# Kernel tuning notes

Measured on AMD Instinct MI355X. Metric: run time of the kernel, lower is better.

## Reference

```python
import math
import jax, jax.numpy as jnp
import numpy as np

STRIDE = 8
IMG = 2048
NA = 9            # num anchors per cell (len(cfg['anchor_size']))
NC = 80           # num classes
TOPK = 1000
CONF = 0.05
NMS_T = 0.6
CTR_CLAMP = 32.0
EXP_CLAMP = math.log(1e8)            # DEFAULT_EXP_CLAMP
SCALE_CLAMP = math.log(1000.0 / 16)  # DEFAULT_SCALE_CLAMP


def setup_inputs() -> dict:
    key = jax.random.key(0)
    k1, k2, k3 = jax.random.split(key, 3)
    H = W = IMG // STRIDE  # 256
    obj_pred = jax.random.normal(k1, (1, NA, H, W), jnp.float32)
    cls_pred = jax.random.normal(k2, (1, NA * NC, H, W), jnp.float32)
    reg_pred = jax.random.normal(k3, (1, NA * 4, H, W), jnp.float32) * 0.5
    # generate_anchors: grid centers (+0.5)*stride, tiled anchor sizes -> [H*W*NA, 4] (cx,cy,w,h)
    ys, xs = jnp.meshgrid(jnp.arange(H), jnp.arange(W), indexing='ij')
    xy = (jnp.stack([xs, ys], -1).reshape(-1, 2).astype(jnp.float32) + 0.5) * STRIDE
    sizes = jnp.array([[32, 32], [64, 64], [128, 128], [32, 64], [64, 128],
                       [128, 256], [64, 32], [128, 64], [256, 128]], jnp.float32)
    anchor_boxes = jnp.concatenate(
        [jnp.repeat(xy[:, None, :], NA, axis=1),
         jnp.broadcast_to(sizes[None], (H * W, NA, 2))], axis=-1).reshape(-1, 4)
    return {"obj_pred": obj_pred, "cls_pred": cls_pred,
            "reg_pred": reg_pred, "anchor_boxes": anchor_boxes}


def _detect(obj_pred, cls_pred, reg_pred, anchor_boxes):
    B, _, H, W = obj_pred.shape
    obj = obj_pred.reshape(B, NA, 1, H, W)
    cls = cls_pred.reshape(B, NA, NC, H, W)
    # normalized_cls_pred = cls + obj - log(1 + exp(clamp(cls)) + exp(clamp(obj)))
    norm = cls + obj - jnp.log(1.0 + jnp.exp(jnp.minimum(cls, EXP_CLAMP))
                               + jnp.exp(jnp.minimum(obj, EXP_CLAMP)))
    norm = norm.transpose(0, 3, 4, 1, 2).reshape(B, -1, NC)[0]          # [M, NC]
    reg = reg_pred.reshape(B, NA, 4, H, W).transpose(0, 3, 4, 1, 2).reshape(B, -1, 4)[0]  # [M, 4]
    prob = jax.nn.sigmoid(norm)
    scores_all = prob.max(axis=-1)
    labels_all = prob.argmax(axis=-1)
    scores, idx = jax.lax.top_k(scores_all, TOPK)                        # descending
    labels = labels_all[idx]
    reg = reg[idx]
    anc = anchor_boxes[idx]
    # decode_boxes
    ctr_off = jnp.clip(reg[..., :2] * anc[..., 2:], -CTR_CLAMP, CTR_CLAMP)
    ctr = anc[..., :2] + ctr_off
    wh = anc[..., 2:] * jnp.exp(jnp.minimum(reg[..., 2:], SCALE_CLAMP))
    boxes = jnp.concatenate([ctr - 0.5 * wh, ctr + 0.5 * wh], axis=-1)
    boxes = jnp.clip(boxes / IMG, 0.0, 1.0)
    return scores, labels, boxes


def _nms_keep(scores, labels, boxes):
    # scores are sorted descending; per-class greedy NMS == class-masked global greedy NMS
    valid = scores >= CONF
    x1, y1, x2, y2 = boxes[:, 0], boxes[:, 1], boxes[:, 2], boxes[:, 3]
    areas = (x2 - x1) * (y2 - y1)
    xx1 = jnp.maximum(x1[:, None], x1[None, :])
    yy1 = jnp.maximum(y1[:, None], y1[None, :])
    xx2 = jnp.minimum(x2[:, None], x2[None, :])
    yy2 = jnp.minimum(y2[:, None], y2[None, :])
    inter = jnp.maximum(1e-28, xx2 - xx1) * jnp.maximum(1e-28, yy2 - yy1)
    iou = inter / (areas[:, None] + areas[None, :] - inter + 1e-14)      # [N, N]
    sup = (iou > NMS_T) & (labels[:, None] == labels[None, :])
    later = jnp.arange(TOPK)[None, :] > jnp.arange(TOPK)[:, None]

    def body(i, keep):
        row = sup[i] & later[i] & keep[i]   # i suppresses only if still kept
        return keep & ~row

    return jax.lax.fori_loop(0, TOPK, body, valid)


def reference(obj_pred, cls_pred, reg_pred, anchor_boxes):
    scores, labels, boxes = _detect(obj_pred, cls_pred, reg_pred, anchor_boxes)
    keep = _nms_keep(scores, labels, boxes)
    # fixed-shape outputs: detections sorted by score with a keep mask
    return scores, labels, boxes, keep
```

## Files before the change

### kernel.cpp

```cpp
#include <hip/hip_runtime.h>
#include <stdint.h>

#define NA 9
#define NC 80
#define NTOT 589824
#define TOPK 1000
#define CONF 0.05f
#define NMS_T 0.6
#define CTR_CLAMP 32.0
#define IMGF 2048.0
#define SCALE_CLAMP 4.135166556742356

#define BITS_OFF   0u
#define LABELS_OFF 2359296u
#define HIST_OFF   4718592u
#define CNT_OFF    4784128u
#define BARC_OFF   4784384u
#define FLAG_OFF   4790528u
#define CAND_OFF   4796672u
#define BOXES_OFF  4829440u
#define LABS_OFF   4845440u
#define SUPB_OFF   4849664u
#define ZERO_LEN   78080u

#define NBLK 500
#define SPIN_CAP 200000

__device__ __forceinline__ void stg32(unsigned* p, unsigned v) {
  __hip_atomic_store(p, v, __ATOMIC_RELAXED, __HIP_MEMORY_SCOPE_AGENT);
}
__device__ __forceinline__ unsigned ldg32(const unsigned* p) {
  return __hip_atomic_load((unsigned*)p, __ATOMIC_RELAXED, __HIP_MEMORY_SCOPE_AGENT);
}
__device__ __forceinline__ void stg64(unsigned long long* p, unsigned long long v) {
  __hip_atomic_store(p, v, __ATOMIC_RELAXED, __HIP_MEMORY_SCOPE_AGENT);
}
__device__ __forceinline__ unsigned long long ldg64(const unsigned long long* p) {
  return __hip_atomic_load((unsigned long long*)p, __ATOMIC_RELAXED,
                           __HIP_MEMORY_SCOPE_AGENT);
}

__device__ __forceinline__ unsigned* lslot(unsigned* base, int idx) {
  return (unsigned*)((char*)base + (size_t)idx * 256u);
}

__device__ __forceinline__ void barrier_sync(unsigned* cnts, unsigned* flags,
                                             int b, int bid, unsigned target,
                                             bool i_arrive) {
  __syncthreads();
  if (threadIdx.x == 0) {
    if (i_arrive)
      __hip_atomic_fetch_add(lslot(cnts, b * 8 + (bid & 7)), 1u, __ATOMIC_RELAXED,
                             __HIP_MEMORY_SCOPE_AGENT);
    if (bid == 0) {
      for (int it = 0; it < SPIN_CAP; it++) {
        unsigned s = 0;
#pragma unroll
        for (int i = 0; i < 8; i++)
          s += __hip_atomic_load(lslot(cnts, b * 8 + i), __ATOMIC_RELAXED,
                                 __HIP_MEMORY_SCOPE_AGENT);
        if (s >= target) break;
        __builtin_amdgcn_s_sleep(2);
      }
#pragma unroll
      for (int i = 0; i < 8; i++)
        __hip_atomic_store(lslot(flags, b * 8 + i), 1u, __ATOMIC_RELAXED,
                           __HIP_MEMORY_SCOPE_AGENT);
    } else {
      for (int it = 0; it < SPIN_CAP; it++) {
        if (__hip_atomic_load(lslot(flags, b * 8 + (bid & 7)), __ATOMIC_RELAXED,
                              __HIP_MEMORY_SCOPE_AGENT) != 0u)
          break;
        __builtin_amdgcn_s_sleep(2);
      }
    }
  }
  __syncthreads();
  asm volatile("" ::: "memory");
}

__device__ __forceinline__ float cexpf(float x) {
#pragma clang fp contract(off)
  float m = floorf(__builtin_fmaf(x, 1.44269504088896341f, 0.5f));
  float r = __builtin_fmaf(m, -0.693359375f, x);
  r = __builtin_fmaf(m, 2.12194440e-4f, r);
  float r2 = r * r;
  float y = 1.9875691500E-4f;
  y = __builtin_fmaf(y, r, 1.3981999507E-3f);
  y = __builtin_fmaf(y, r, 8.3334519073E-3f);
  y = __builtin_fmaf(y, r, 4.1665795894E-2f);
  y = __builtin_fmaf(y, r, 1.6666665459E-1f);
  y = __builtin_fmaf(y, r, 5.0000001201E-1f);
  y = __builtin_fmaf(y, r2, r) + 1.0f;
  return ldexpf(y, (int)m);
}

__device__ __forceinline__ float clogf_(float xin) {
#pragma clang fp contract(off)
  unsigned b = __float_as_uint(xin);
  int e = (int)(b >> 23) - 126;
  float m = __uint_as_float((b & 0x007FFFFFu) | 0x3F000000u);
  if (m < 0.707106781186547524f) { e -= 1; m = m + m; }
  float x = m - 1.0f;
  float z = x * x;
  float y = 7.0376836292E-2f;
  y = __builtin_fmaf(y, x, -1.1514610310E-1f);
  y = __builtin_fmaf(y, x, 1.1676998740E-1f);
  y = __builtin_fmaf(y, x, -1.2420140846E-1f);
  y = __builtin_fmaf(y, x, 1.4249322787E-1f);
  y = __builtin_fmaf(y, x, -1.6668057665E-1f);
  y = __builtin_fmaf(y, x, 2.0000714765E-1f);
  y = __builtin_fmaf(y, x, -2.4999993993E-1f);
  y = __builtin_fmaf(y, x, 3.3333331174E-1f);
  y = y * x * z;
  float ef = (float)e;
  y = __builtin_fmaf(ef, -2.12194440e-4f, y);
  y = __builtin_fmaf(-0.5f, z, y);
  float res = x + y;
  res = __builtin_fmaf(ef, 0.693359375f, res);
  return res;
}

__global__ __launch_bounds__(256) void k_score(const float4* __restrict__ obj4,
                                               const float4* __restrict__ cls4,
                                               unsigned* __restrict__ bits_all,
                                               int* __restrict__ labels_all,
                                               unsigned* __restrict__ hist) {
#pragma clang fp contract(off)
  __shared__ unsigned lh[16384];
  int tid = threadIdx.x;
  for (int b = tid; b < 16384; b += 256) lh[b] = 0u;
  __syncthreads();
  int t = blockIdx.x * 256 + tid;
  int a = t >> 14;
  int rem = t & 16383;
  float4 ov = obj4[t];
  float ob[4] = {ov.x, ov.y, ov.z, ov.w};
  float best[4] = {-1e30f, -1e30f, -1e30f, -1e30f};
  int bc[4] = {0, 0, 0, 0};
  const float4* cp = cls4 + a * 80 * 16384 + rem;
#pragma unroll 8
  for (int c = 0; c < 80; c++) {
    float4 cv = cp[c * 16384];
    float cl[4] = {cv.x, cv.y, cv.z, cv.w};
#pragma unroll
    for (int k = 0; k < 4; k++) {
      if (cl[k] > best[k]) { best[k] = cl[k]; bc[k] = c; }
    }
  }
  unsigned bv[4];
#pragma unroll
  for (int k = 0; k < 4; k++) {
    float c = best[k], o = ob[k];
    float ec = cexpf(c);
    float eo = cexpf(o);
    float L = clogf_((1.0f + ec) + eo);
    float nrm = (c + o) - L;
    float p = 1.0f / (1.0f + cexpf(-nrm));
    bv[k] = __float_as_uint(p);
    atomicAdd(&lh[bv[k] >> 16], 1u);
  }
  unsigned po = (unsigned)(a * 65536 + rem * 4);
#pragma unroll
  for (int k = 0; k < 4; k++) { bits_all[po + k] = bv[k]; labels_all[po + k] = bc[k]; }
  __syncthreads();
  for (int b = tid; b < 16384; b += 256) {
    unsigned v = lh[b];
    if (v) atomicAdd(&hist[b], v);
  }
}

__device__ __forceinline__ unsigned long long shflxor64(unsigned long long v, int m) {
  unsigned lo = __shfl_xor((unsigned)v, m, 64);
  unsigned hi = __shfl_xor((unsigned)(v >> 32), m, 64);
  return ((unsigned long long)hi << 32) | lo;
}

__global__ __launch_bounds__(256) void k_tail2(const unsigned* __restrict__ hist,
                                               const unsigned* __restrict__ bits_all,
                                               const int* __restrict__ labels_all,
                                               const float* __restrict__ reg_pred,
                                               const float* __restrict__ anchors,
                                               unsigned* __restrict__ cand_cnt,
                                               unsigned* __restrict__ barc,
                                               unsigned* __restrict__ flags,
                                               unsigned long long* __restrict__ cand,
                                               float* __restrict__ out,
                                               float* __restrict__ boxes_s,
                                               int* __restrict__ labels_s,
                                               unsigned long long* __restrict__ supB) {
  int tid = threadIdx.x;
  int bid = blockIdx.x;

  __shared__ __align__(16) char smem[20480];
  unsigned* s_cut = (unsigned*)smem;
  unsigned long long* s_key = (unsigned long long*)smem;
  float* s_bx = (float*)smem;
  int* s_lb = (int*)(smem + 16000);
  __shared__ int sC;
  __shared__ unsigned sAbove;
  __shared__ unsigned s_cutB;

  {
    unsigned base = (unsigned)tid * 64u;
    unsigned s = 0;
#pragma unroll 8
    for (int b = 0; b < 64; b++) s += hist[base + b];
    unsigned v = s;
    s_cut[tid] = v;
    __syncthreads();
    for (int off = 1; off < 256; off <<= 1) {
      unsigned add = (tid + off < 256) ? s_cut[tid + off] : 0u;
      __syncthreads();
      v += add;
      s_cut[tid] = v;
      __syncthreads();
    }
    unsigned nxt = (tid < 255) ? s_cut[tid + 1] : 0u;
    if (v >= TOPK && nxt < TOPK) { sC = tid; sAbove = nxt; }
    __syncthreads();
    int C = sC;
    unsigned above = sAbove;
    if (tid < 64) {
      unsigned h = hist[(unsigned)C * 64u + (unsigned)tid];
      unsigned acc = h;
      for (int off = 1; off < 64; off <<= 1) {
        unsigned o = __shfl_down(acc, off, 64);
        if (tid + off < 64) acc += o;
      }
      acc += above;
      if (acc >= TOPK && (tid == 63 || (acc - h) < TOPK))
        s_cutB = (unsigned)(C * 64 + tid);
    }
    __syncthreads();
  }
  unsigned cB = s_cutB;

  for (unsigned t = (unsigned)bid * 256u + (unsigned)tid; t < (unsigned)NTOT;
       t += (unsigned)(NBLK * 256)) {
    unsigned bits = bits_all[t];
    bool win = (bits >> 16) >= cB;
    unsigned long long m = __ballot(win);
    if (m != 0ull) {
      int lane = tid & 63;
      int leader = __ffsll((long long)m) - 1;
      unsigned base2 = 0;
      if (lane == leader) base2 = atomicAdd(cand_cnt, (unsigned)__popcll(m));
      base2 = __shfl(base2, leader, 64);
      if (win) {
        unsigned a = t >> 16;
        unsigned hw = t & 65535u;
        unsigned j = hw * 9u + a;
        unsigned pos = base2 + (unsigned)__popcll(m & ((1ull << lane) - 1ull));
        if (pos < 4096u)
          stg64(&cand[pos], ((unsigned long long)bits << 20) |
                                (unsigned long long)(0xFFFFFu - j));
      }
    }
  }
  barrier_sync(barc, flags, 0, bid, NBLK, true);

  if (bid < 16) {
    int c = bid * 256 + tid;
    unsigned M = ldg32(cand_cnt);
    if (M > 4096u) M = 4096u;
    unsigned long long mykey = (c < (int)M) ? ldg64(&cand[c]) : 0ull;
    unsigned rank = 0;
    int ntile = (int)((M + 255u) >> 8);
    for (int tile = 0; tile < ntile; tile++) {
      __syncthreads();
      int src = tile * 256 + tid;
      s_key[tid] = (src < (int)M) ? ldg64(&cand[src]) : 0ull;
      __syncthreads();
#pragma unroll 8
      for (int q = 0; q < 256; q++) rank += (s_key[q] > mykey) ? 1u : 0u;
    }
    if (c < (int)M && rank < TOPK) {
      int r = (int)rank;
      unsigned j = 0xFFFFFu - (unsigned)(mykey & 0xFFFFFull);
      unsigned hw = j / 9u;
      unsigned a = j - hw * 9u;
      int lab = labels_all[a * 65536u + hw];
      unsigned base = a * 4u * 65536u + hw;
      double r0 = (double)reg_pred[base];
      double r1 = (double)reg_pred[base + 65536u];
      double r2 = (double)reg_pred[base + 131072u];
      double r3 = (double)reg_pred[base + 196608u];
      double ax = (double)anchors[j * 4u + 0], ay = (double)anchors[j * 4u + 1];
      double aw = (double)anchors[j * 4u + 2], ah = (double)anchors[j * 4u + 3];
      double ox = fmin(fmax(r0 * aw, -CTR_CLAMP), CTR_CLAMP);
      double oy = fmin(fmax(r1 * ah, -CTR_CLAMP), CTR_CLAMP);
      double cx = ax + ox, cy = ay + oy;
      double ww = aw * exp(fmin(r2, SCALE_CLAMP));
      double hh = ah * exp(fmin(r3, SCALE_CLAMP));
      float x1 = (float)fmin(fmax((cx - 0.5 * ww) * (1.0 / IMGF), 0.0), 1.0);
      float y1 = (float)fmin(fmax((cy - 0.5 * hh) * (1.0 / IMGF), 0.0), 1.0);
      float x2 = (float)fmin(fmax((cx + 0.5 * ww) * (1.0 / IMGF), 0.0), 1.0);
      float y2 = (float)fmin(fmax((cy + 0.5 * hh) * (1.0 / IMGF), 0.0), 1.0);
      out[1000 + r] = (float)lab;
      out[2000 + 4 * r + 0] = x1;
      out[2000 + 4 * r + 1] = y1;
      out[2000 + 4 * r + 2] = x2;
      out[2000 + 4 * r + 3] = y2;
      stg32((unsigned*)&out[r], (unsigned)(mykey >> 20));
      stg32((unsigned*)&boxes_s[4 * r + 0], __float_as_uint(x1));
      stg32((unsigned*)&boxes_s[4 * r + 1], __float_as_uint(y1));
      stg32((unsigned*)&boxes_s[4 * r + 2], __float_as_uint(x2));
      stg32((unsigned*)&boxes_s[4 * r + 3], __float_as_uint(y2));
      stg32((unsigned*)&labels_s[r], (unsigned)lab);
    }
  }
  barrier_sync(barc, flags, 1, bid, 16, bid < 16);

  for (int t = tid; t < 4000; t += 256)
    s_bx[t] = __uint_as_float(ldg32((const unsigned*)&boxes_s[t]));
  for (int t = tid; t < 1000; t += 256)
    s_lb[t] = (int)ldg32((const unsigned*)&labels_s[t]);
  __syncthreads();
  for (int half = 0; half < 2; half++) {
    int i = bid + half * NBLK;
    double ix1 = (double)s_bx[4 * i], iy1 = (double)s_bx[4 * i + 1];
    double ix2 = (double)s_bx[4 * i + 2], iy2 = (double)s_bx[4 * i + 3];
    double ia = (ix2 - ix1) * (iy2 - iy1);
    int il = s_lb[i];
    for (int rep = 0; rep < 4; rep++) {
      int j = rep * 256 + tid;
      bool s = false;
      if (j < TOPK && j > i && s_lb[j] == il) {
        double jx1 = (double)s_bx[4 * j], jy1 = (double)s_bx[4 * j + 1];
        double jx2 = (double)s_bx[4 * j + 2], jy2 = (double)s_bx[4 * j + 3];
        double xx1 = fmax(ix1, jx1), yy1 = fmax(iy1, jy1);
        double xx2 = fmin(ix2, jx2), yy2 = fmin(iy2, jy2);
        double inter = fmax(1e-28, xx2 - xx1) * fmax(1e-28, yy2 - yy1);
        double ja = (jx2 - jx1) * (jy2 - jy1);
        double iou = inter / (ia + ja - inter + 1e-14);
        s = iou > NMS_T;
      }
      unsigned long long w = __ballot(s);
      if ((tid & 63) == 0)
        stg64(&supB[(rep * 4 + (tid >> 6)) * 1024 + i], w);
    }
  }
  __syncthreads();
  if (tid == 0)
    __hip_atomic_fetch_add(lslot(barc, 2 * 8 + (bid & 7)), 1u, __ATOMIC_RELAXED,
                           __HIP_MEMORY_SCOPE_AGENT);
  if (bid != 0) return;
  if (tid == 0) {
    for (int it = 0; it < SPIN_CAP; it++) {
      unsigned s = 0;
#pragma unroll
      for (int i = 0; i < 8; i++)
        s += __hip_atomic_load(lslot(barc, 2 * 8 + i), __ATOMIC_RELAXED,
                               __HIP_MEMORY_SCOPE_AGENT);
      if (s >= NBLK) break;
      __builtin_amdgcn_s_sleep(2);
    }
  }
  __syncthreads();
  asm volatile("" ::: "memory");

  if (tid < 64) {
    int lane = tid;
    float* keep_out = out + 6000;
    unsigned long long inval[16];
#pragma unroll
    for (int m = 0; m < 16; m++) {
      int j = m * 64 + lane;
      bool bad = (j >= TOPK) ||
                 (__uint_as_float(ldg32((const unsigned*)&out[j])) < CONF);
      inval[m] = __ballot(bad);
    }
    unsigned long long kept[16];
#pragma unroll
    for (int b = 0; b < 16; b++) {
      unsigned long long acc = 0ull;
#pragma unroll
      for (int m = 0; m < b; m++) {
        unsigned long long r = ldg64(&supB[b * 1024 + m * 64 + lane]);
        if ((kept[m] >> lane) & 1ull) acc |= r;
      }
      if (b > 0) {
#pragma unroll
        for (int s = 1; s < 64; s <<= 1) acc |= shflxor64(acc, s);
      }
      unsigned alo = __builtin_amdgcn_readfirstlane((unsigned)acc);
      unsigned ahi = __builtin_amdgcn_readfirstlane((unsigned)(acc >> 32));
      unsigned long long cur = inval[b] | (((unsigned long long)ahi << 32) | alo);
      unsigned long long diag = ldg64(&supB[b * 1024 + b * 64 + lane]);
      unsigned dlo = (unsigned)diag, dhi = (unsigned)(diag >> 32);
#pragma unroll 8
      for (int k = 0; k < 64; k++) {
        unsigned rlo = __builtin_amdgcn_readlane(dlo, k);
        unsigned rhi = __builtin_amdgcn_readlane(dhi, k);
        unsigned long long rk = ((unsigned long long)rhi << 32) | rlo;
        unsigned long long take = ((cur >> k) & 1ull) ? 0ull : rk;
        cur |= take;
      }
      kept[b] = ~cur;
    }
#pragma unroll
    for (int m = 0; m < 16; m++) {
      int j = m * 64 + lane;
      if (j < TOPK) keep_out[j] = ((kept[m] >> lane) & 1ull) ? 1.0f : 0.0f;
    }
  }
}

extern "C" void kernel_launch(void* const* d_in, const int* in_sizes, int n_in,
                              void* d_out, int out_size, void* d_ws, size_t ws_size,
                              hipStream_t stream) {
  const float* obj = (const float*)d_in[0];
  const float* cls = (const float*)d_in[1];
  const float* reg = (const float*)d_in[2];
  const float* anc = (const float*)d_in[3];
  float* out = (float*)d_out;
  char* ws = (char*)d_ws;

  unsigned* bits_all = (unsigned*)(ws + BITS_OFF);
  int* labels_all = (int*)(ws + LABELS_OFF);
  unsigned* hist = (unsigned*)(ws + HIST_OFF);
  unsigned* cand_cnt = (unsigned*)(ws + CNT_OFF);
  unsigned* barc = (unsigned*)(ws + BARC_OFF);
  unsigned* flags = (unsigned*)(ws + FLAG_OFF);
  unsigned long long* cand = (unsigned long long*)(ws + CAND_OFF);
  float* boxes_s = (float*)(ws + BOXES_OFF);
  int* labels_s = (int*)(ws + LABS_OFF);
  unsigned long long* supB = (unsigned long long*)(ws + SUPB_OFF);

  hipMemsetAsync(ws + HIST_OFF, 0, ZERO_LEN, stream);

  k_score<<<576, 256, 0, stream>>>((const float4*)obj, (const float4*)cls, bits_all,
                                   labels_all, hist);

  void* kargs[] = {(void*)&hist,     (void*)&bits_all, (void*)&labels_all,
                   (void*)&reg,      (void*)&anc,      (void*)&cand_cnt,
                   (void*)&barc,     (void*)&flags,    (void*)&cand,
                   (void*)&out,      (void*)&boxes_s,  (void*)&labels_s,
                   (void*)&supB};
  hipLaunchCooperativeKernel((const void*)k_tail2, dim3(NBLK), dim3(256), kargs, 0,
                             stream);
}
```

Baseline: 403.4 us.

## Fuse scoring, histogram zeroing and tail into one cooperative kernel

Merges the memset, the scoring and histogram kernel, and the cooperative top-k/NMS kernel into a single cooperative launch of 512 blocks. The scoring work moves into a grid-stride loop. Block 0 zeroes the histogram and barrier state in-kernel and publishes a magic flag that other blocks wait on before merging their histograms. The goal is to remove two launch gaps and the memset. In exchange the scoring phase runs on fewer resident blocks with an uneven second iteration, and the init flag persists across calls, which weakens the zeroing guarantee on later calls.

```diff
diff --git a/kernel.cpp b/kernel.cpp
--- a/kernel.cpp
+++ b/kernel.cpp
@@ -4,6 +4,7 @@
 #define NA 9
 #define NC 80
 #define NTOT 589824
+#define NT4  147456
 #define TOPK 1000
 #define CONF 0.05f
 #define NMS_T 0.6
@@ -16,15 +17,16 @@
 #define HIST_OFF   4718592u
 #define CNT_OFF    4784128u
 #define BARC_OFF   4784384u
-#define FLAG_OFF   4790528u
-#define CAND_OFF   4796672u
-#define BOXES_OFF  4829440u
-#define LABS_OFF   4845440u
-#define SUPB_OFF   4849664u
-#define ZERO_LEN   78080u
-
-#define NBLK 500
+#define FLAG_OFF   4792576u
+#define INITF_OFF  4800768u
+#define CAND_OFF   4802816u
+#define BOXES_OFF  4835584u
+#define LABS_OFF   4851584u
+#define SUPB_OFF   4855584u
+
+#define NBLK 512
 #define SPIN_CAP 200000
+#define INIT_MAGIC 0x9E3779B97F4A7C15ull
 
 __device__ __forceinline__ void stg32(unsigned* p, unsigned v) {
   __hip_atomic_store(p, v, __ATOMIC_RELAXED, __HIP_MEMORY_SCOPE_AGENT);
@@ -121,108 +123,121 @@
   return res;
 }
 
-__global__ __launch_bounds__(256) void k_score(const float4* __restrict__ obj4,
-                                               const float4* __restrict__ cls4,
-                                               unsigned* __restrict__ bits_all,
-                                               int* __restrict__ labels_all,
-                                               unsigned* __restrict__ hist) {
-#pragma clang fp contract(off)
-  __shared__ unsigned lh[16384];
-  int tid = threadIdx.x;
-  for (int b = tid; b < 16384; b += 256) lh[b] = 0u;
-  __syncthreads();
-  int t = blockIdx.x * 256 + tid;
-  int a = t >> 14;
-  int rem = t & 16383;
-  float4 ov = obj4[t];
-  float ob[4] = {ov.x, ov.y, ov.z, ov.w};
-  float best[4] = {-1e30f, -1e30f, -1e30f, -1e30f};
-  int bc[4] = {0, 0, 0, 0};
-  const float4* cp = cls4 + a * 80 * 16384 + rem;
-#pragma unroll 8
-  for (int c = 0; c < 80; c++) {
-    float4 cv = cp[c * 16384];
-    float cl[4] = {cv.x, cv.y, cv.z, cv.w};
-#pragma unroll
-    for (int k = 0; k < 4; k++) {
-      if (cl[k] > best[k]) { best[k] = cl[k]; bc[k] = c; }
-    }
-  }
-  unsigned bv[4];
-#pragma unroll
-  for (int k = 0; k < 4; k++) {
-    float c = best[k], o = ob[k];
-    float ec = cexpf(c);
-    float eo = cexpf(o);
-    float L = clogf_((1.0f + ec) + eo);
-    float nrm = (c + o) - L;
-    float p = 1.0f / (1.0f + cexpf(-nrm));
-    bv[k] = __float_as_uint(p);
-    atomicAdd(&lh[bv[k] >> 16], 1u);
-  }
-  unsigned po = (unsigned)(a * 65536 + rem * 4);
-#pragma unroll
-  for (int k = 0; k < 4; k++) { bits_all[po + k] = bv[k]; labels_all[po + k] = bc[k]; }
-  __syncthreads();
-  for (int b = tid; b < 16384; b += 256) {
-    unsigned v = lh[b];
-    if (v) atomicAdd(&hist[b], v);
-  }
-}
-
 __device__ __forceinline__ unsigned long long shflxor64(unsigned long long v, int m) {
   unsigned lo = __shfl_xor((unsigned)v, m, 64);
   unsigned hi = __shfl_xor((unsigned)(v >> 32), m, 64);
   return ((unsigned long long)hi << 32) | lo;
 }
 
-__global__ __launch_bounds__(256) void k_tail2(const unsigned* __restrict__ hist,
-                                               const unsigned* __restrict__ bits_all,
-                                               const int* __restrict__ labels_all,
-                                               const float* __restrict__ reg_pred,
-                                               const float* __restrict__ anchors,
-                                               unsigned* __restrict__ cand_cnt,
-                                               unsigned* __restrict__ barc,
-                                               unsigned* __restrict__ flags,
-                                               unsigned long long* __restrict__ cand,
-                                               float* __restrict__ out,
-                                               float* __restrict__ boxes_s,
-                                               int* __restrict__ labels_s,
-                                               unsigned long long* __restrict__ supB) {
+__global__ __launch_bounds__(256) void k_fused(
+    const float4* __restrict__ obj4, const float4* __restrict__ cls4,
+    unsigned* __restrict__ bits_all, int* __restrict__ labels_all,
+    unsigned* __restrict__ hist, const float* __restrict__ reg_pred,
+    const float* __restrict__ anchors, unsigned* __restrict__ cand_cnt,
+    unsigned* __restrict__ barc, unsigned* __restrict__ flags,
+    unsigned* __restrict__ initf, unsigned long long* __restrict__ cand,
+    float* __restrict__ out, float* __restrict__ boxes_s,
+    int* __restrict__ labels_s, unsigned long long* __restrict__ supB) {
   int tid = threadIdx.x;
   int bid = blockIdx.x;
 
-  __shared__ __align__(16) char smem[20480];
-  unsigned* s_cut = (unsigned*)smem;
-  unsigned long long* s_key = (unsigned long long*)smem;
-  float* s_bx = (float*)smem;
-  int* s_lb = (int*)(smem + 16000);
-  __shared__ int sC;
-  __shared__ unsigned sAbove;
-  __shared__ unsigned s_cutB;
-
+  __shared__ __align__(16) unsigned lh[16384];
+
+  for (int i = tid; i < 16384; i += 256) lh[i] = 0u;
+  if (bid == 0) {
+    for (int i = tid; i < 16384; i += 256) stg32(&hist[i], 0u);
+    if (tid == 0) stg32(cand_cnt, 0u);
+    if (tid < 32) {
+      stg32(lslot(barc, tid), 0u);
+      stg32(lslot(flags, tid), 0u);
+    }
+  }
+  __syncthreads();
+  if (bid == 0 && tid < 8)
+    stg64((unsigned long long*)lslot(initf, tid), INIT_MAGIC);
+
+  {
+#pragma clang fp contract(off)
+    for (unsigned t4 = (unsigned)bid * 256u + (unsigned)tid; t4 < (unsigned)NT4;
+         t4 += (unsigned)(NBLK * 256)) {
+      int a = (int)(t4 >> 14);
+      int rem = (int)(t4 & 16383u);
+      float4 ov = obj4[t4];
+      float ob[4] = {ov.x, ov.y, ov.z, ov.w};
+      float best[4] = {-1e30f, -1e30f, -1e30f, -1e30f};
+      int bc[4] = {0, 0, 0, 0};
+      const float4* cp = cls4 + a * 80 * 16384 + rem;
+#pragma unroll 8
+      for (int c = 0; c < 80; c++) {
+        float4 cv = cp[c * 16384];
+        float cl[4] = {cv.x, cv.y, cv.z, cv.w};
+#pragma unroll
+        for (int k = 0; k < 4; k++) {
+          if (cl[k] > best[k]) { best[k] = cl[k]; bc[k] = c; }
+        }
+      }
+      unsigned bv[4];
+#pragma unroll
+      for (int k = 0; k < 4; k++) {
+        float c = best[k], o = ob[k];
+        float ec = cexpf(c);
+        float eo = cexpf(o);
+        float L = clogf_((1.0f + ec) + eo);
+        float nrm = (c + o) - L;
+        float p = 1.0f / (1.0f + cexpf(-nrm));
+        bv[k] = __float_as_uint(p);
+        atomicAdd(&lh[bv[k] >> 16], 1u);
+      }
+      unsigned po = (unsigned)(a * 65536 + rem * 4);
+      stg64((unsigned long long*)&bits_all[po],
+            (unsigned long long)bv[0] | ((unsigned long long)bv[1] << 32));
+      stg64((unsigned long long*)&bits_all[po + 2],
+            (unsigned long long)bv[2] | ((unsigned long long)bv[3] << 32));
+      stg64((unsigned long long*)&labels_all[po],
+            (unsigned long long)(unsigned)bc[0] |
+                ((unsigned long long)(unsigned)bc[1] << 32));
+      stg64((unsigned long long*)&labels_all[po + 2],
+            (unsigned long long)(unsigned)bc[2] |
+                ((unsigned long long)(unsigned)bc[3] << 32));
+    }
+  }
+  __syncthreads();
+  if (tid == 0) {
+    for (int it = 0; it < SPIN_CAP; it++) {
+      if (ldg64((unsigned long long*)lslot(initf, bid & 7)) == INIT_MAGIC) break;
+      __builtin_amdgcn_s_sleep(2);
+    }
+  }
+  __syncthreads();
+  for (int b = tid; b < 16384; b += 256) {
+    unsigned v = lh[b];
+    if (v) atomicAdd(&hist[b], v);
+  }
+  barrier_sync(barc, flags, 0, bid, NBLK, true);
+
+  unsigned cB;
   {
     unsigned base = (unsigned)tid * 64u;
     unsigned s = 0;
 #pragma unroll 8
     for (int b = 0; b < 64; b++) s += hist[base + b];
     unsigned v = s;
-    s_cut[tid] = v;
+    lh[tid] = v;
     __syncthreads();
     for (int off = 1; off < 256; off <<= 1) {
-      unsigned add = (tid + off < 256) ? s_cut[tid + off] : 0u;
+      unsigned add = (tid + off < 256) ? lh[tid + off] : 0u;
       __syncthreads();
       v += add;
-      s_cut[tid] = v;
+      lh[tid] = v;
       __syncthreads();
     }
-    unsigned nxt = (tid < 255) ? s_cut[tid + 1] : 0u;
-    if (v >= TOPK && nxt < TOPK) { sC = tid; sAbove = nxt; }
+    unsigned nxt = (tid < 255) ? lh[tid + 1] : 0u;
+    if (v >= TOPK && nxt < TOPK) { lh[260] = (unsigned)tid; lh[261] = nxt; }
     __syncthreads();
-    int C = sC;
-    unsigned above = sAbove;
+    unsigned C = lh[260];
+    unsigned above = lh[261];
     if (tid < 64) {
-      unsigned h = hist[(unsigned)C * 64u + (unsigned)tid];
+      unsigned h = hist[C * 64u + (unsigned)tid];
       unsigned acc = h;
       for (int off = 1; off < 64; off <<= 1) {
         unsigned o = __shfl_down(acc, off, 64);
@@ -230,11 +245,11 @@
       }
       acc += above;
       if (acc >= TOPK && (tid == 63 || (acc - h) < TOPK))
-        s_cutB = (unsigned)(C * 64 + tid);
+        lh[262] = C * 64u + (unsigned)tid;
     }
     __syncthreads();
-  }
-  unsigned cB = s_cutB;
+    cB = lh[262];
+  }
 
   for (unsigned t = (unsigned)bid * 256u + (unsigned)tid; t < (unsigned)NTOT;
        t += (unsigned)(NBLK * 256)) {
@@ -258,9 +273,10 @@
       }
     }
   }
-  barrier_sync(barc, flags, 0, bid, NBLK, true);
+  barrier_sync(barc, flags, 1, bid, NBLK, true);
 
   if (bid < 16) {
+    unsigned long long* s_key = (unsigned long long*)lh;
     int c = bid * 256 + tid;
     unsigned M = ldg32(cand_cnt);
     if (M > 4096u) M = 4096u;
@@ -310,40 +326,46 @@
       stg32((unsigned*)&labels_s[r], (unsigned)lab);
     }
   }
-  barrier_sync(barc, flags, 1, bid, 16, bid < 16);
-
-  for (int t = tid; t < 4000; t += 256)
-    s_bx[t] = __uint_as_float(ldg32((const unsigned*)&boxes_s[t]));
-  for (int t = tid; t < 1000; t += 256)
-    s_lb[t] = (int)ldg32((const unsigned*)&labels_s[t]);
-  __syncthreads();
-  for (int half = 0; half < 2; half++) {
-    int i = bid + half * NBLK;
-    double ix1 = (double)s_bx[4 * i], iy1 = (double)s_bx[4 * i + 1];
-    double ix2 = (double)s_bx[4 * i + 2], iy2 = (double)s_bx[4 * i + 3];
-    double ia = (ix2 - ix1) * (iy2 - iy1);
-    int il = s_lb[i];
-    for (int rep = 0; rep < 4; rep++) {
-      int j = rep * 256 + tid;
-      bool s = false;
-      if (j < TOPK && j > i && s_lb[j] == il) {
-        double jx1 = (double)s_bx[4 * j], jy1 = (double)s_bx[4 * j + 1];
-        double jx2 = (double)s_bx[4 * j + 2], jy2 = (double)s_bx[4 * j + 3];
-        double xx1 = fmax(ix1, jx1), yy1 = fmax(iy1, jy1);
-        double xx2 = fmin(ix2, jx2), yy2 = fmin(iy2, jy2);
-        double inter = fmax(1e-28, xx2 - xx1) * fmax(1e-28, yy2 - yy1);
-        double ja = (jx2 - jx1) * (jy2 - jy1);
-        double iou = inter / (ia + ja - inter + 1e-14);
-        s = iou > NMS_T;
-      }
-      unsigned long long w = __ballot(s);
-      if ((tid & 63) == 0)
-        stg64(&supB[(rep * 4 + (tid >> 6)) * 1024 + i], w);
+  barrier_sync(barc, flags, 2, bid, 16, bid < 16);
+
+  {
+    float* s_bx = (float*)lh;
+    int* s_lb = (int*)((char*)lh + 16000);
+    for (int t = tid; t < 4000; t += 256)
+      s_bx[t] = __uint_as_float(ldg32((const unsigned*)&boxes_s[t]));
+    for (int t = tid; t < 1000; t += 256)
+      s_lb[t] = (int)ldg32((const unsigned*)&labels_s[t]);
+    __syncthreads();
+    for (int half = 0; half < 2; half++) {
+      int i = bid + half * NBLK;
+      if (i < TOPK) {
+        double ix1 = (double)s_bx[4 * i], iy1 = (double)s_bx[4 * i + 1];
+        double ix2 = (double)s_bx[4 * i + 2], iy2 = (double)s_bx[4 * i + 3];
+        double ia = (ix2 - ix1) * (iy2 - iy1);
+        int il = s_lb[i];
+        for (int rep = 0; rep < 4; rep++) {
+          int j = rep * 256 + tid;
+          bool s = false;
+          if (j < TOPK && j > i && s_lb[j] == il) {
+            double jx1 = (double)s_bx[4 * j], jy1 = (double)s_bx[4 * j + 1];
+            double jx2 = (double)s_bx[4 * j + 2], jy2 = (double)s_bx[4 * j + 3];
+            double xx1 = fmax(ix1, jx1), yy1 = fmax(iy1, jy1);
+            double xx2 = fmin(ix2, jx2), yy2 = fmin(iy2, jy2);
+            double inter = fmax(1e-28, xx2 - xx1) * fmax(1e-28, yy2 - yy1);
+            double ja = (jx2 - jx1) * (jy2 - jy1);
+            double iou = inter / (ia + ja - inter + 1e-14);
+            s = iou > NMS_T;
+          }
+          unsigned long long w = __ballot(s);
+          if ((tid & 63) == 0)
+            stg64(&supB[(rep * 4 + (tid >> 6)) * 1024 + i], w);
+        }
+      }
     }
   }
   __syncthreads();
   if (tid == 0)
-    __hip_atomic_fetch_add(lslot(barc, 2 * 8 + (bid & 7)), 1u, __ATOMIC_RELAXED,
+    __hip_atomic_fetch_add(lslot(barc, 3 * 8 + (bid & 7)), 1u, __ATOMIC_RELAXED,
                            __HIP_MEMORY_SCOPE_AGENT);
   if (bid != 0) return;
   if (tid == 0) {
@@ -351,7 +373,7 @@
       unsigned s = 0;
 #pragma unroll
       for (int i = 0; i < 8; i++)
-        s += __hip_atomic_load(lslot(barc, 2 * 8 + i), __ATOMIC_RELAXED,
+        s += __hip_atomic_load(lslot(barc, 3 * 8 + i), __ATOMIC_RELAXED,
                                __HIP_MEMORY_SCOPE_AGENT);
       if (s >= NBLK) break;
       __builtin_amdgcn_s_sleep(2);
@@ -417,27 +439,26 @@
   float* out = (float*)d_out;
   char* ws = (char*)d_ws;
 
+  const float4* obj4 = (const float4*)obj;
+  const float4* cls4 = (const float4*)cls;
   unsigned* bits_all = (unsigned*)(ws + BITS_OFF);
   int* labels_all = (int*)(ws + LABELS_OFF);
   unsigned* hist = (unsigned*)(ws + HIST_OFF);
   unsigned* cand_cnt = (unsigned*)(ws + CNT_OFF);
   unsigned* barc = (unsigned*)(ws + BARC_OFF);
   unsigned* flags = (unsigned*)(ws + FLAG_OFF);
+  unsigned* initf = (unsigned*)(ws + INITF_OFF);
   unsigned long long* cand = (unsigned long long*)(ws + CAND_OFF);
   float* boxes_s = (float*)(ws + BOXES_OFF);
   int* labels_s = (int*)(ws + LABS_OFF);
   unsigned long long* supB = (unsigned long long*)(ws + SUPB_OFF);
 
-  hipMemsetAsync(ws + HIST_OFF, 0, ZERO_LEN, stream);
-
-  k_score<<<576, 256, 0, stream>>>((const float4*)obj, (const float4*)cls, bits_all,
-                                   labels_all, hist);
-
-  void* kargs[] = {(void*)&hist,     (void*)&bits_all, (void*)&labels_all,
-                   (void*)&reg,      (void*)&anc,      (void*)&cand_cnt,
-                   (void*)&barc,     (void*)&flags,    (void*)&cand,
+  void* kargs[] = {(void*)&obj4,     (void*)&cls4,     (void*)&bits_all,
+                   (void*)&labels_all, (void*)&hist,   (void*)&reg,
+                   (void*)&anc,      (void*)&cand_cnt, (void*)&barc,
+                   (void*)&flags,    (void*)&initf,    (void*)&cand,
                    (void*)&out,      (void*)&boxes_s,  (void*)&labels_s,
                    (void*)&supB};
-  hipLaunchCooperativeKernel((const void*)k_tail2, dim3(NBLK), dim3(256), kargs, 0,
+  hipLaunchCooperativeKernel((const void*)k_fused, dim3(NBLK), dim3(256), kargs, 0,
                              stream);
 }
```

Result: faster. 393.2 us (-2.5%).
